# Optimization experiments

Hardware: AMD Instinct MI355X
Metric: run time of the kernel (lower is better)

Reference implementation:

```python
import jax, jax.numpy as jnp
import numpy as np
import math

PATCH = 9
C_IN = 128
C_FEAT = 128
B, H, W = 32, 96, 96


def setup_inputs() -> dict:
    key = jax.random.key(0)
    k1, k2, k3 = jax.random.split(key, 3)
    input1 = jax.random.normal(k1, (B, C_IN, H, W), dtype=jnp.float32)
    input2 = jax.random.normal(k2, (B, C_IN, H, W), dtype=jnp.float32)
    # 1x1 conv params (kernel_size=1 -> weight is effectively [C_out, C_in])
    proj_w = jax.random.normal(k3, (C_FEAT, C_IN), dtype=jnp.float32) / math.sqrt(C_IN)
    proj_b = jnp.zeros((C_FEAT,), dtype=jnp.float32)
    return {"input1": input1, "input2": input2, "proj_w": proj_w, "proj_b": proj_b}


def _proj(x, w, b):
    # 1x1 conv == per-pixel channel mixing
    return jnp.einsum('bchw,fc->bfhw', x, w) + b[None, :, None, None]


def reference(input1, input2, proj_w, proj_b):
    x1 = _proj(input1, proj_w, proj_b)          # [B, F, H, W]
    x2 = _proj(input2, proj_w, proj_b)          # [B, F, H, W]
    r = PATCH // 2
    h, w = x1.shape[-2:]
    x2p = jnp.pad(x2, ((0, 0), (0, 0), (r, r), (r, r)))  # zero-pad borders
    # Cost volume: for each displacement (di, dj) in the PATCH x PATCH window,
    # sum over channels of x1[.,.,i,j] * x2[.,.,i+di-r, j+dj-r].
    corrs = []
    for di in range(PATCH):
        for dj in range(PATCH):
            shifted = x2p[:, :, di:di + h, dj:dj + w]
            corrs.append(jnp.einsum('bchw,bchw->bhw', x1, shifted))
    out = jnp.stack(corrs, axis=1)              # [B, PATCH*PATCH, H, W]
    return out / math.sqrt(C_FEAT)
```

## Files before the change

### kernel.cpp

```cpp
#include <hip/hip_runtime.h>
#include <stdint.h>

#define B_   32
#define CIN  128
#define HH   96
#define WW   96
#define HW   (HH*WW)
#define NPIX (B_*HW)
#define AROWS 144
#define APAD  136
#define SCALE 0.08838834764831845f
#define ESW   98

#define AB_OFF 0u
#define V_OFF  36864u
#define S_OFF  37376u
#define Y2_OFF 40960u
#define Z2_OFF (Y2_OFF + 75497472u)
#define ZP_OFF (Z2_OFF + 1179648u)
#define WS_NEED (ZP_OFF + 16384u)

typedef __attribute__((ext_vector_type(8))) short bf16x8;
typedef __attribute__((ext_vector_type(4))) float f32x4;

__device__ inline unsigned short f2bf(float f) {
    unsigned int u = __float_as_uint(f);
    u += 0x7fffu + ((u >> 16) & 1u);
    return (unsigned short)(u >> 16);
}

__device__ inline int bswz(int row, int byteoff) {
    return row * 128 + (byteoff ^ (((row ^ (row >> 3)) & 7) << 4));
}

__global__ __launch_bounds__(128) void k1_prep(
    const float* __restrict__ Wm, const float* __restrict__ bias,
    unsigned short* __restrict__ Abuf, float* __restrict__ vbuf,
    float* __restrict__ sbuf, char* __restrict__ zp) {
    int r = blockIdx.x;
    int c = threadIdx.x;
    int gid = r * 128 + c;
    if (gid < 1024)
        *(uint4*)(zp + gid * 16) = make_uint4(0u, 0u, 0u, 0u);

    float acc = 0.f;
    if (r < 128) {
        for (int f = 0; f < 128; ++f)
            acc += Wm[f * 128 + r] * Wm[f * 128 + c];
    } else if (r == 128) {
        for (int f = 0; f < 128; ++f)
            acc += Wm[f * 128 + c] * bias[f];
        vbuf[c] = acc;
        if (c == 0) {
            float s = 0.f;
            for (int f = 0; f < 128; ++f) s += bias[f] * bias[f];
            sbuf[0] = s;
        }
    }
    Abuf[r * 128 + c] = f2bf(acc);
}

__global__ __launch_bounds__(512, 4) void k2_proj(
    const float* __restrict__ a2, const unsigned short* __restrict__ Abuf,
    const float* __restrict__ vbuf, const float* __restrict__ sbuf,
    unsigned short* __restrict__ y2, float* __restrict__ z2) {
    __shared__ __align__(16) unsigned short Asm[AROWS * APAD];
    __shared__ __align__(128) unsigned char Bsm[2][128 * 128];

    const int t = threadIdx.x;
    const int tile = blockIdx.x;
    const int b = tile / 72;
    const int hw0 = (tile - b * 72) * 128;

    for (int i = t; i < 2304; i += 512) {
        int row = i >> 4, seg = i & 15;
        *(uint4*)(&Asm[row * APAD + seg * 8]) =
            *(const uint4*)(Abuf + row * 128 + seg * 8);
    }

    {
        const int pxq = t & 31;
        const int ctp = t >> 5;
        const float* a2b = a2 + (size_t)b * (CIN * HW) + hw0 + pxq * 4;
#pragma unroll
        for (int it = 0; it < 4; ++it) {
            const int cc0 = (ctp + it * 16) * 2;
            float4 f0 = *(const float4*)(a2b + (size_t)cc0 * HW);
            float4 f1 = *(const float4*)(a2b + (size_t)(cc0 + 1) * HW);
            unsigned char* pl = Bsm[cc0 >> 6];
            const int bo = (cc0 & 63) * 2;
            float a0[4] = {f0.x, f0.y, f0.z, f0.w};
            float a1[4] = {f1.x, f1.y, f1.z, f1.w};
#pragma unroll
            for (int r = 0; r < 4; ++r) {
                unsigned int pk = (unsigned int)f2bf(a0[r]) |
                                  ((unsigned int)f2bf(a1[r]) << 16);
                *(unsigned int*)(&pl[bswz(pxq * 4 + r, bo)]) = pk;
            }
        }
    }
    __syncthreads();

    const int wv = t >> 6;
    const int l = t & 63;
    const int li = l & 15;
    const int hi = l >> 4;
    const int rbase = hi * 4;
    const int pxl = wv * 16 + li;

    bf16x8 bfr[4];
#pragma unroll
    for (int kk = 0; kk < 4; ++kk) {
        const int k0 = kk * 32 + hi * 8;
        bfr[kk] = *(const bf16x8*)(&Bsm[k0 >> 6][bswz(pxl, (k0 & 63) * 2)]);
    }

    f32x4 acc[9];
#pragma unroll
    for (int m = 0; m < 9; ++m) acc[m] = (f32x4){0.f, 0.f, 0.f, 0.f};

#pragma unroll
    for (int kk = 0; kk < 4; ++kk) {
        const int k0 = kk * 32 + hi * 8;
#pragma unroll
        for (int m = 0; m < 9; ++m) {
            bf16x8 af = *(const bf16x8*)(&Asm[(m * 16 + li) * APAD + k0]);
            acc[m] = __builtin_amdgcn_mfma_f32_16x16x32_bf16(af, bfr[kk], acc[m], 0, 0, 0);
        }
    }

    const int px = hw0 + pxl;
    const size_t pxoff = (size_t)b * HW + px;
#pragma unroll
    for (int m = 0; m < 8; ++m) {
        int c0 = m * 16 + rbase;
        ushort4 pk;
        pk.x = f2bf(acc[m].x + vbuf[c0 + 0]);
        pk.y = f2bf(acc[m].y + vbuf[c0 + 1]);
        pk.z = f2bf(acc[m].z + vbuf[c0 + 2]);
        pk.w = f2bf(acc[m].w + vbuf[c0 + 3]);
        *(ushort4*)(y2 + ((size_t)(c0 >> 3) * NPIX + pxoff) * 8 + (c0 & 7)) = pk;
    }
    if (rbase == 0) {
        z2[pxoff] = acc[8].x + sbuf[0];
    }
}

__global__ __launch_bounds__(256, 2) void k3_corr(
    const float* __restrict__ x1, const char* __restrict__ wsb,
    float* __restrict__ out) {
    __shared__ __align__(128) unsigned char EX[49152];
    unsigned short* Es16 = (unsigned short*)EX;

    const int t = threadIdx.x;
    const int lid = blockIdx.x;
    const int T = (lid & 7) * 192 + (lid >> 3);
    const int b = T / 48;
    const int h = (T - b * 48) * 2;

    const int wv = t >> 6;
    const int l = t & 63;
    const int li = l & 15;
    const int hi = l >> 4;

    {
        const float* x1b = x1 + (size_t)b * (CIN * HW) + (size_t)h * 96;
#pragma unroll
        for (int im = 0; im < 2; ++im) {
            const float* xr = x1b + im * 96;
#pragma unroll
            for (int it = 0; it < 6; ++it) {
                int idx = t + it * 256;
                int ccp = idx / 24;
                int pxq = idx - ccp * 24;
                int cc0 = ccp * 2;
                float4 f0 = *(const float4*)(xr + (size_t)cc0 * HW + pxq * 4);
                float4 f1 = *(const float4*)(xr + (size_t)(cc0 + 1) * HW + pxq * 4);
                unsigned char* pl = EX + im * 24576 + (cc0 >> 6) * 12288;
                const int bo = (cc0 & 63) * 2;
                float a0[4] = {f0.x, f0.y, f0.z, f0.w};
                float a1[4] = {f1.x, f1.y, f1.z, f1.w};
#pragma unroll
                for (int r = 0; r < 4; ++r) {
                    unsigned int pk = (unsigned int)f2bf(a0[r]) |
                                      ((unsigned int)f2bf(a1[r]) << 16);
                    *(unsigned int*)(&pl[bswz(pxq * 4 + r, bo)]) = pk;
                }
            }
        }
    }

    unsigned offb[12];
#pragma unroll
    for (int cc = 0; cc < 4; ++cc)
#pragma unroll
        for (int g = 0; g < 3; ++g) {
            const int pxj = (wv * 3 + g) * 8 + li - 4;
            long off;
            if ((unsigned)pxj < 96u)
                off = (long)Y2_OFF +
                      ((long)(cc * 4 + hi) * NPIX + (long)b * HW +
                       (long)(h - 4) * 96 + pxj) * 16;
            else
                off = (long)ZP_OFF;
            offb[cc * 3 + g] = (unsigned)off;
        }

    int offz[3];
#pragma unroll
    for (int g = 0; g < 3; ++g) {
        const int zc = (wv * 3 + g) * 8 + li - 4;
        offz[g] = ((unsigned)zc < 96u)
            ? (int)Z2_OFF + (b * HW + (h - 4) * 96 + zc) * 4
            : (int)ZP_OFF;
    }

    const int imw = hi >> 1;

    __syncthreads();

    bf16x8 afr[3][4];
    {
        const int imA = li >> 3;
        const int pA = li & 7;
#pragma unroll
        for (int g = 0; g < 3; ++g) {
            const int px = (wv * 3 + g) * 8 + pA;
#pragma unroll
            for (int cc = 0; cc < 4; ++cc) {
                const int k0 = cc * 32 + hi * 8;
                afr[g][cc] = *(const bf16x8*)(
                    &EX[imA * 24576 + (k0 >> 6) * 12288 + bswz(px, (k0 & 63) * 2)]);
            }
        }
    }
    __syncthreads();

    uint4 pv[2][12];
#pragma unroll
    for (int q = 0; q < 12; ++q)
        pv[0][q] = *(const uint4*)(wsb + offb[q]);
#pragma unroll
    for (int q = 0; q < 12; ++q)
        pv[1][q] = *(const uint4*)(wsb + offb[q] + 1536);

    float zvc[2][3];
#pragma unroll
    for (int r0 = 0; r0 < 2; ++r0) {
        const int zok = ((unsigned)(h - 4 + r0) < 96u);
#pragma unroll
        for (int g = 0; g < 3; ++g)
            zvc[r0][g] = *(const float*)(wsb + (zok ? offz[g] + r0 * 384
                                                    : (int)ZP_OFF));
    }

#pragma unroll
    for (int di = 0; di < 10; ++di) {
        const int cur = di & 1;
        const int hs = h - 4 + di;
        const int zrowok = ((unsigned)hs < 96u);

        f32x4 ac[3];
#pragma unroll
        for (int g = 0; g < 3; ++g) ac[g] = (f32x4){0.f, 0.f, 0.f, 0.f};

        if (zrowok) {
#pragma unroll
            for (int cc = 0; cc < 4; ++cc)
#pragma unroll
                for (int g = 0; g < 3; ++g) {
                    union { uint4 u; bf16x8 f; } cv;
                    cv.u = pv[cur][cc * 3 + g];
                    ac[g] = __builtin_amdgcn_mfma_f32_16x16x32_bf16(
                        afr[g][cc], cv.f, ac[g], 0, 0, 0);
                }
        }

        if (di < 8) {
#pragma unroll
            for (int q = 0; q < 12; ++q)
                pv[cur][q] = *(const uint4*)(wsb + offb[q] + (di + 2) * 1536);
        }

        {
            const int rnd = di - imw;
            if ((unsigned)rnd < 9u) {
#pragma unroll
                for (int g = 0; g < 3; ++g) {
                    const int uu = wv * 3 + g;
#pragma unroll
                    for (int reg = 0; reg < 4; ++reg) {
                        const int ip = (hi & 1) * 4 + reg;
                        const int dji = li - ip;
                        if (dji >= 0 && dji <= 8)
                            Es16[(imw * 81 + rnd * 9 + dji) * ESW + uu * 8 + ip] =
                                f2bf((ac[g][reg] + zvc[cur][g]) * SCALE);
                    }
                }
            }
        }

        if (di < 8) {
            const int zokn = ((unsigned)(hs + 2) < 96u);
#pragma unroll
            for (int g = 0; g < 3; ++g)
                zvc[cur][g] = *(const float*)(wsb + (zokn ? offz[g] + (di + 2) * 384
                                                          : (int)ZP_OFF));
        }
    }

    __syncthreads();
    const size_t obase = (size_t)b * 81 * HW + (size_t)h * 96;
    for (int idx = t; idx < 7776; idx += 256) {
        const int p = idx / 3888;
        const int r2 = idx - p * 3888;
        const int s = r2 / 48, w2 = r2 - s * 48;
        unsigned u = *(const unsigned*)(&Es16[(p * 81 + s) * ESW + w2 * 2]);
        float2 fv;
        fv.x = __uint_as_float(u << 16);
        fv.y = __uint_as_float(u & 0xffff0000u);
        *(float2*)(&out[obase + (size_t)s * HW + p * 96 + w2 * 2]) = fv;
    }
}

extern "C" void kernel_launch(void* const* d_in, const int* in_sizes, int n_in,
                              void* d_out, int out_size, void* d_ws, size_t ws_size,
                              hipStream_t stream) {
    const float* input1 = (const float*)d_in[0];
    const float* input2 = (const float*)d_in[1];
    const float* proj_w = (const float*)d_in[2];
    const float* proj_b = (const float*)d_in[3];
    float* out = (float*)d_out;

    char* ws = (char*)d_ws;
    if (ws_size < WS_NEED) return;

    unsigned short* Abuf = (unsigned short*)(ws + AB_OFF);
    float* vbuf = (float*)(ws + V_OFF);
    float* sbuf = (float*)(ws + S_OFF);
    unsigned short* y2 = (unsigned short*)(ws + Y2_OFF);
    float* z2 = (float*)(ws + Z2_OFF);
    char* zp = ws + ZP_OFF;

    k1_prep<<<dim3(144), dim3(128), 0, stream>>>(proj_w, proj_b, Abuf, vbuf, sbuf, zp);
    k2_proj<<<dim3(2304), dim3(512), 0, stream>>>(input2, Abuf, vbuf, sbuf, y2, z2);
    k3_corr<<<dim3(1536), dim3(256), 0, stream>>>(input1, ws, out);
}
```

Measured before the change: 153.4 us.

## Process four output rows per correlation block to reuse loaded x2 rows

The correlation kernel now handles four output rows per block instead of two, halving the grid to 768 blocks. Each streamed x2 projection row is fed to MFMAs for two row pairs, so global loads of y2/z2 per output row are cut. The costs are more registers (two sets of A fragments and accumulators), a larger LDS staging buffer near 62KB that may limit occupancy, and fewer blocks to fill the GPU.

```diff
diff --git a/kernel.cpp b/kernel.cpp
--- a/kernel.cpp
+++ b/kernel.cpp
@@ -149,22 +149,50 @@
 __global__ __launch_bounds__(256, 2) void k3_corr(
     const float* __restrict__ x1, const char* __restrict__ wsb,
     float* __restrict__ out) {
-    __shared__ __align__(128) unsigned char EX[49152];
+    __shared__ __align__(128) unsigned char EX[63552];
     unsigned short* Es16 = (unsigned short*)EX;
 
     const int t = threadIdx.x;
     const int lid = blockIdx.x;
-    const int T = (lid & 7) * 192 + (lid >> 3);
-    const int b = T / 48;
-    const int h = (T - b * 48) * 2;
+    const int T = (lid & 7) * 96 + (lid >> 3);
+    const int b = T / 24;
+    const int h0 = (T - b * 24) * 4;
 
     const int wv = t >> 6;
     const int l = t & 63;
     const int li = l & 15;
     const int hi = l >> 4;
-
-    {
-        const float* x1b = x1 + (size_t)b * (CIN * HW) + (size_t)h * 96;
+    const int imw = hi >> 1;
+
+    unsigned offb[12];
+#pragma unroll
+    for (int cc = 0; cc < 4; ++cc)
+#pragma unroll
+        for (int g = 0; g < 3; ++g) {
+            const int pxj = (wv * 3 + g) * 8 + li - 4;
+            long off;
+            if ((unsigned)pxj < 96u)
+                off = (long)Y2_OFF +
+                      ((long)(cc * 4 + hi) * NPIX + (long)b * HW +
+                       (long)(h0 - 4) * 96 + pxj) * 16;
+            else
+                off = (long)ZP_OFF;
+            offb[cc * 3 + g] = (unsigned)off;
+        }
+
+    int offz[3];
+#pragma unroll
+    for (int g = 0; g < 3; ++g) {
+        const int zc = (wv * 3 + g) * 8 + li - 4;
+        offz[g] = ((unsigned)zc < 96u)
+            ? (int)Z2_OFF + (b * HW + (h0 - 4) * 96 + zc) * 4
+            : (int)ZP_OFF;
+    }
+
+    bf16x8 afr[2][3][4];
+#pragma unroll
+    for (int tt = 0; tt < 2; ++tt) {
+        const float* x1b = x1 + (size_t)b * (CIN * HW) + (size_t)(h0 + 2 * tt) * 96;
 #pragma unroll
         for (int im = 0; im < 2; ++im) {
             const float* xr = x1b + im * 96;
@@ -188,53 +216,23 @@
                 }
             }
         }
-    }
-
-    unsigned offb[12];
-#pragma unroll
-    for (int cc = 0; cc < 4; ++cc)
-#pragma unroll
-        for (int g = 0; g < 3; ++g) {
-            const int pxj = (wv * 3 + g) * 8 + li - 4;
-            long off;
-            if ((unsigned)pxj < 96u)
-                off = (long)Y2_OFF +
-                      ((long)(cc * 4 + hi) * NPIX + (long)b * HW +
-                       (long)(h - 4) * 96 + pxj) * 16;
-            else
-                off = (long)ZP_OFF;
-            offb[cc * 3 + g] = (unsigned)off;
-        }
-
-    int offz[3];
-#pragma unroll
-    for (int g = 0; g < 3; ++g) {
-        const int zc = (wv * 3 + g) * 8 + li - 4;
-        offz[g] = ((unsigned)zc < 96u)
-            ? (int)Z2_OFF + (b * HW + (h - 4) * 96 + zc) * 4
-            : (int)ZP_OFF;
-    }
-
-    const int imw = hi >> 1;
-
-    __syncthreads();
-
-    bf16x8 afr[3][4];
-    {
-        const int imA = li >> 3;
-        const int pA = li & 7;
-#pragma unroll
-        for (int g = 0; g < 3; ++g) {
-            const int px = (wv * 3 + g) * 8 + pA;
-#pragma unroll
-            for (int cc = 0; cc < 4; ++cc) {
-                const int k0 = cc * 32 + hi * 8;
-                afr[g][cc] = *(const bf16x8*)(
-                    &EX[imA * 24576 + (k0 >> 6) * 12288 + bswz(px, (k0 & 63) * 2)]);
+        __syncthreads();
+        {
+            const int imA = li >> 3;
+            const int pA = li & 7;
+#pragma unroll
+            for (int g = 0; g < 3; ++g) {
+                const int px = (wv * 3 + g) * 8 + pA;
+#pragma unroll
+                for (int cc = 0; cc < 4; ++cc) {
+                    const int k0 = cc * 32 + hi * 8;
+                    afr[tt][g][cc] = *(const bf16x8*)(
+                        &EX[imA * 24576 + (k0 >> 6) * 12288 + bswz(px, (k0 & 63) * 2)]);
+                }
             }
         }
-    }
-    __syncthreads();
+        __syncthreads();
+    }
 
     uint4 pv[2][12];
 #pragma unroll
@@ -244,25 +242,22 @@
     for (int q = 0; q < 12; ++q)
         pv[1][q] = *(const uint4*)(wsb + offb[q] + 1536);
 
-    float zvc[2][3];
-#pragma unroll
-    for (int r0 = 0; r0 < 2; ++r0) {
-        const int zok = ((unsigned)(h - 4 + r0) < 96u);
+#pragma unroll
+    for (int di = 0; di < 12; ++di) {
+        const int cur = di & 1;
+        const int hs = h0 - 4 + di;
+        const int zrowok = ((unsigned)hs < 96u);
+        float zv[3];
 #pragma unroll
         for (int g = 0; g < 3; ++g)
-            zvc[r0][g] = *(const float*)(wsb + (zok ? offz[g] + r0 * 384
-                                                    : (int)ZP_OFF));
-    }
-
-#pragma unroll
-    for (int di = 0; di < 10; ++di) {
-        const int cur = di & 1;
-        const int hs = h - 4 + di;
-        const int zrowok = ((unsigned)hs < 96u);
-
-        f32x4 ac[3];
-#pragma unroll
-        for (int g = 0; g < 3; ++g) ac[g] = (f32x4){0.f, 0.f, 0.f, 0.f};
+            zv[g] = *(const float*)(wsb + (zrowok ? offz[g] + di * 384
+                                                  : (int)ZP_OFF));
+
+        f32x4 ac[2][3];
+#pragma unroll
+        for (int tt = 0; tt < 2; ++tt)
+#pragma unroll
+            for (int g = 0; g < 3; ++g) ac[tt][g] = (f32x4){0.f, 0.f, 0.f, 0.f};
 
         if (zrowok) {
 #pragma unroll
@@ -271,19 +266,24 @@
                 for (int g = 0; g < 3; ++g) {
                     union { uint4 u; bf16x8 f; } cv;
                     cv.u = pv[cur][cc * 3 + g];
-                    ac[g] = __builtin_amdgcn_mfma_f32_16x16x32_bf16(
-                        afr[g][cc], cv.f, ac[g], 0, 0, 0);
+                    if (di <= 9)
+                        ac[0][g] = __builtin_amdgcn_mfma_f32_16x16x32_bf16(
+                            afr[0][g][cc], cv.f, ac[0][g], 0, 0, 0);
+                    if (di >= 2)
+                        ac[1][g] = __builtin_amdgcn_mfma_f32_16x16x32_bf16(
+                            afr[1][g][cc], cv.f, ac[1][g], 0, 0, 0);
                 }
         }
 
-        if (di < 8) {
+        if (di < 10) {
 #pragma unroll
             for (int q = 0; q < 12; ++q)
                 pv[cur][q] = *(const uint4*)(wsb + offb[q] + (di + 2) * 1536);
         }
 
-        {
-            const int rnd = di - imw;
+#pragma unroll
+        for (int tt = 0; tt < 2; ++tt) {
+            const int rnd = di - 2 * tt - imw;
             if ((unsigned)rnd < 9u) {
 #pragma unroll
                 for (int g = 0; g < 3; ++g) {
@@ -293,25 +293,17 @@
                         const int ip = (hi & 1) * 4 + reg;
                         const int dji = li - ip;
                         if (dji >= 0 && dji <= 8)
-                            Es16[(imw * 81 + rnd * 9 + dji) * ESW + uu * 8 + ip] =
-                                f2bf((ac[g][reg] + zvc[cur][g]) * SCALE);
+                            Es16[((tt * 2 + imw) * 81 + rnd * 9 + dji) * ESW + uu * 8 + ip] =
+                                f2bf((ac[tt][g][reg] + zv[g]) * SCALE);
                     }
                 }
             }
         }
-
-        if (di < 8) {
-            const int zokn = ((unsigned)(hs + 2) < 96u);
-#pragma unroll
-            for (int g = 0; g < 3; ++g)
-                zvc[cur][g] = *(const float*)(wsb + (zokn ? offz[g] + (di + 2) * 384
-                                                          : (int)ZP_OFF));
-        }
     }
 
     __syncthreads();
-    const size_t obase = (size_t)b * 81 * HW + (size_t)h * 96;
-    for (int idx = t; idx < 7776; idx += 256) {
+    const size_t obase = (size_t)b * 81 * HW + (size_t)h0 * 96;
+    for (int idx = t; idx < 15552; idx += 256) {
         const int p = idx / 3888;
         const int r2 = idx - p * 3888;
         const int s = r2 / 48, w2 = r2 - s * 48;
@@ -344,5 +336,5 @@
 
     k1_prep<<<dim3(144), dim3(128), 0, stream>>>(proj_w, proj_b, Abuf, vbuf, sbuf, zp);
     k2_proj<<<dim3(2304), dim3(512), 0, stream>>>(input2, Abuf, vbuf, sbuf, y2, z2);
-    k3_corr<<<dim3(1536), dim3(256), 0, stream>>>(input1, ws, out);
-}
+    k3_corr<<<dim3(768), dim3(256), 0, stream>>>(input1, ws, out);
+}
```

Measured after the change: 214.7 us. 39.9% more time.
